# Kernel tuning notes

Measured on AMD Instinct MI355X. Metric: run time of the kernel, lower is better.

The kernel has to match this reference:

```python
import jax, jax.numpy as jnp
import numpy as np

B, S, H = 2, 4096, 1024
WINDOW = 32


def setup_inputs() -> dict:
    key = jax.random.key(0)
    ks = jax.random.split(key, 10)
    s = 1.0 / np.sqrt(H)
    return {
        "hidden_states": jax.random.normal(ks[0], (B, S, H), dtype=jnp.float32),
        "Wq": jax.random.normal(ks[1], (H, H), dtype=jnp.float32) * s,
        "Wk": jax.random.normal(ks[2], (H, H), dtype=jnp.float32) * s,
        "Wv": jax.random.normal(ks[3], (H, H), dtype=jnp.float32) * s,
        "Wo": jax.random.normal(ks[4], (H, H), dtype=jnp.float32) * s,
        "ln_w": jnp.ones((H,), dtype=jnp.float32),
        "ln_b": jnp.zeros((H,), dtype=jnp.float32),
        "W1": jax.random.normal(ks[5], (H // 2, H), dtype=jnp.float32) * s,
        "b1": jnp.zeros((H // 2,), dtype=jnp.float32),
        "W2": jax.random.normal(ks[6], (H, H // 2), dtype=jnp.float32) * (1.0 / np.sqrt(H // 2)),
        "b2": jnp.zeros((H,), dtype=jnp.float32),
    }


def _layernorm(x, w, b, eps=1e-5):
    mu = jnp.mean(x, axis=-1, keepdims=True)
    var = jnp.var(x, axis=-1, keepdims=True)
    return (x - mu) * jax.lax.rsqrt(var + eps) * w + b


def reference(hidden_states, Wq, Wk, Wv, Wo, ln_w, ln_b, W1, b1, W2, b2):
    x = hidden_states  # [B,S,H]
    q = x @ Wq.T
    k = x @ Wk.T
    v = x @ Wv.T
    # banded causal mask: keep j<=i and j >= i-WINDOW+1
    i = jnp.arange(S)[:, None]
    j = jnp.arange(S)[None, :]
    local_mask = (j <= i) & (j >= i - WINDOW + 1)  # [S,S] bool
    scores = jnp.einsum('bqh,bkh->bqk', q, k) / np.sqrt(H)
    scores = jnp.where(local_mask[None], scores, -jnp.inf)
    probs = jax.nn.softmax(scores, axis=-1)
    attn_out = jnp.einsum('bqk,bkh->bqh', probs, v) @ Wo.T
    draft = x + attn_out
    h = _layernorm(draft, ln_w, ln_b)
    h = jax.nn.gelu(h @ W1.T + b1, approximate=False)
    adapter_out = h @ W2.T + b2
    return draft + adapter_out
```

## Files before the change

kernel.cpp:

```cpp
#include <hip/hip_runtime.h>
#include <stdint.h>

typedef unsigned short u16;
typedef __bf16 bfx8 __attribute__((ext_vector_type(8)));
typedef float f32x4 __attribute__((ext_vector_type(4)));

__device__ __forceinline__ u16 f2bf(float x) {
    unsigned int u = __float_as_uint(x);
    u += 0x7fffu + ((u >> 16) & 1u);
    return (u16)(u >> 16);
}

__device__ __forceinline__ void async16(const void* g, void* l) {
    __builtin_amdgcn_global_load_lds(
        (const __attribute__((address_space(1))) unsigned int*)(uintptr_t)g,
        (__attribute__((address_space(3))) unsigned int*)(unsigned int)(uintptr_t)l,
        16, 0, 0);
}

#define S_BARRIER() asm volatile("s_barrier" ::: "memory")
#define WAIT_VM6() asm volatile("s_waitcnt vmcnt(6)" ::: "memory")
#define WAIT_VM8() asm volatile("s_waitcnt vmcnt(8)" ::: "memory")
#define WAIT_VM0() asm volatile("s_waitcnt vmcnt(0)" ::: "memory")

struct CastArgs {
    const float* src[7];
    u16* dst[7];
    int nblk[7];
};
__global__ __launch_bounds__(256) void cast_all(CastArgs a) {
    int b = blockIdx.x, seg = 0;
    while (b >= a.nblk[seg]) { b -= a.nblk[seg]; ++seg; }
    int i = b * 256 + threadIdx.x;
    const float4* p = (const float4*)(a.src[seg] + (size_t)i * 8);
    float4 x = p[0], y = p[1];
    ushort4 o0, o1;
    o0.x = f2bf(x.x); o0.y = f2bf(x.y); o0.z = f2bf(x.z); o0.w = f2bf(x.w);
    o1.x = f2bf(y.x); o1.y = f2bf(y.y); o1.z = f2bf(y.z); o1.w = f2bf(y.w);
    ushort4* q = (ushort4*)(a.dst[seg] + (size_t)i * 8);
    q[0] = o0; q[1] = o1;
}

#define QKV_LDA(SLOT, RBASE)                                                  \
    {                                                                         \
        _Pragma("unroll") for (int m = 0; m < 4; ++m) {                       \
            int r = (RBASE) + m * 16 + laneR;                                 \
            int ph = (laneK + (r >> 2)) & 3;                                  \
            af[m] = *(const bfx8*)(lds + (SLOT) + r * 64 + ph * 16);          \
        }                                                                     \
    }
#define QKV_LDB(SLOT)                                                         \
    {                                                                         \
        _Pragma("unroll") for (int n = 0; n < 4; ++n) {                       \
            int r = bBase + n * 16 + laneR;                                   \
            int ph = (laneK + (r >> 2)) & 3;                                  \
            bf[n] = *(const bfx8*)(lds + (SLOT) + r * 64 + ph * 16);          \
        }                                                                     \
    }
#define QKV_MFMA(Q)                                                           \
    __builtin_amdgcn_s_setprio(1);                                            \
    _Pragma("unroll") for (int m = 0; m < 4; ++m)                             \
        _Pragma("unroll") for (int n = 0; n < 4; ++n)                         \
            acc[(Q) + m][n] = __builtin_amdgcn_mfma_f32_16x16x32_bf16(        \
                af[m], bf[n], acc[(Q) + m][n], 0, 0, 0);                      \
    __builtin_amdgcn_s_setprio(0);

__global__ __launch_bounds__(512, 2)
void gemm_qkv(const u16* __restrict__ A, const u16* __restrict__ Bw,
              u16* __restrict__ outq, u16* __restrict__ outk,
              u16* __restrict__ vt, int K) {
    __shared__ __align__(1024) unsigned char lds[131072];
    const int t = threadIdx.x;
    const int lane = t & 63;
    const int w = t >> 6;
    const int laneR = lane & 15, laneK = lane >> 4;
    const int wm = w >> 2, wn = w & 3;
    const int b = blockIdx.x;
    const int swz = (b & 7) * 48 + (b >> 3);
    const int row0 = (swz / 12) * 256;
    const int col0 = (swz % 12) * 256;
    const int nt = K >> 6;

    const int c0 = t, c1 = 512 + t;
    const u16* pA0 = A + (size_t)(row0 + (c0 >> 2)) * K + (((c0 & 3) - (c0 >> 4)) & 3) * 8;
    const u16* pA1 = A + (size_t)(row0 + (c1 >> 2)) * K + (((c1 & 3) - (c1 >> 4)) & 3) * 8;
    const u16* pB0 = Bw + (size_t)(col0 + (c0 >> 2)) * K + (((c0 & 3) - (c0 >> 4)) & 3) * 8;
    const u16* pB1 = Bw + (size_t)(col0 + (c1 >> 2)) * K + (((c1 & 3) - (c1 >> 4)) & 3) * 8;
    const unsigned dst0 = (unsigned)c0 * 16u, dst1 = (unsigned)c1 * 16u;

    auto stageA = [&](int d, int ks, int tk) {
        unsigned base = (unsigned)d * 65536u + (unsigned)ks * 16384u;
        async16(pA0 + tk * 64 + ks * 32, lds + base + dst0);
        async16(pA1 + tk * 64 + ks * 32, lds + base + dst1);
    };
    auto stageB = [&](int d, int ks, int tk) {
        unsigned base = (unsigned)d * 65536u + 32768u + (unsigned)ks * 16384u;
        async16(pB0 + tk * 64 + ks * 32, lds + base + dst0);
        async16(pB1 + tk * 64 + ks * 32, lds + base + dst1);
    };

    stageA(0, 0, 0); stageB(0, 0, 0);
    stageA(0, 1, 0); stageB(0, 1, 0);
    stageA(1, 0, 1); stageB(1, 0, 1);
    WAIT_VM8();
    S_BARRIER();

    f32x4 acc[8][4] = {};
    const int aRow = wm * 128;
    const int bBase = wn * 64;

    for (int tk = 0; tk < nt; ++tk) {
        const unsigned d = (unsigned)(tk & 1) * 65536u;
        const int t1 = (tk + 1 < nt) ? tk + 1 : nt - 1;
        const int t2 = (tk + 2 < nt) ? tk + 2 : nt - 1;
        bfx8 af[4], bf[4];
        QKV_LDA(d, aRow)
        QKV_LDB(d + 32768u)
        stageA(t1 & 1, 1, t1);
        S_BARRIER();
        QKV_MFMA(0)
        S_BARRIER();
        QKV_LDA(d, aRow + 64)
        stageB(t1 & 1, 1, t1);
        S_BARRIER();
        QKV_MFMA(4)
        WAIT_VM8();
        S_BARRIER();
        QKV_LDA(d + 16384u, aRow)
        QKV_LDB(d + 49152u)
        stageA(t2 & 1, 0, t2);
        S_BARRIER();
        QKV_MFMA(0)
        S_BARRIER();
        QKV_LDA(d + 16384u, aRow + 64)
        stageB(t2 & 1, 0, t2);
        S_BARRIER();
        QKV_MFMA(4)
        WAIT_VM8();
        S_BARRIER();
    }
    WAIT_VM0();

    const int colsec = col0 >> 10;
#pragma unroll
    for (int mi = 0; mi < 8; ++mi) {
        const int gr0 = row0 + wm * 128 + mi * 16 + laneK * 4;
#pragma unroll
        for (int n = 0; n < 4; ++n) {
            const int gc = col0 + wn * 64 + n * 16 + laneR;
            if (colsec == 0) {
#pragma unroll
                for (int r = 0; r < 4; ++r)
                    outq[(size_t)(gr0 + r) * 1024 + gc] = f2bf(acc[mi][n][r]);
            } else if (colsec == 1) {
#pragma unroll
                for (int r = 0; r < 4; ++r)
                    outk[(size_t)(gr0 + r) * 1024 + (gc - 1024)] = f2bf(acc[mi][n][r]);
            } else {
                ushort4 o4;
                o4.x = f2bf(acc[mi][n][0]); o4.y = f2bf(acc[mi][n][1]);
                o4.z = f2bf(acc[mi][n][2]); o4.w = f2bf(acc[mi][n][3]);
                *(ushort4*)(vt + (((size_t)(gr0 >> 12)) * 1024 + (gc - 2048)) * 4096 +
                            (gr0 & 4095)) = o4;
            }
        }
    }
}

template <int EPI>
__global__ __launch_bounds__(512, 2)
void gemm_nt(const u16* __restrict__ A, const u16* __restrict__ Bw,
             u16* __restrict__ outb, float* __restrict__ outf,
             const float* __restrict__ res, const float* __restrict__ bias,
             int M, int N, int K) {
    __shared__ __align__(1024) unsigned char lds[147456];
    const int t = threadIdx.x;
    const int lane = t & 63, w = t >> 6;
    const int laneR = lane & 15, laneK = lane >> 4;
    const int wr = w >> 1, wc = w & 1;
    const int row0 = blockIdx.y * 256, col0 = blockIdx.x * 128;
    const int nt = K >> 6;

    f32x4 acc[4][4] = {};

    const u16* srcA[4];
    const u16* srcB[2];
    unsigned dA[4], dB[2];
#pragma unroll
    for (int i = 0; i < 4; ++i) {
        int li = i * 512 + t;
        int row = li >> 3, ko = li & 7;
        srcA[i] = A + (size_t)(row0 + row) * K + (ko ^ (row & 7)) * 8;
        dA[i] = li * 16;
    }
#pragma unroll
    for (int i = 0; i < 2; ++i) {
        int li = i * 512 + t;
        int row = li >> 3, ko = li & 7;
        srcB[i] = Bw + (size_t)(col0 + row) * K + (ko ^ (row & 7)) * 8;
        dB[i] = 32768 + li * 16;
    }

    auto stage = [&](int b, int tk, int h) {
        unsigned char* base = lds + b * 49152;
        const int o = tk * 64;
        if (h == 0) {
            async16(srcA[0] + o, base + dA[0]);
            async16(srcA[1] + o, base + dA[1]);
            async16(srcB[0] + o, base + dB[0]);
        } else {
            async16(srcA[2] + o, base + dA[2]);
            async16(srcA[3] + o, base + dA[3]);
            async16(srcB[1] + o, base + dB[1]);
        }
    };

    stage(0, 0, 0); stage(0, 0, 1);
    stage(1, 1, 0); stage(1, 1, 1);

    for (int tk = 0; tk < nt; ++tk) {
        unsigned char* bufA = lds + (tk % 3) * 49152;
        unsigned char* bufB = bufA + 32768;
        if (tk + 1 < nt) { WAIT_VM6(); } else { WAIT_VM0(); }
        S_BARRIER();
        const bool pf = (tk + 2 < nt);
        const int nb = (tk + 2) % 3;
#pragma unroll
        for (int ks = 0; ks < 2; ++ks) {
            bfx8 af[4], bf[4];
#pragma unroll
            for (int m = 0; m < 4; ++m) {
                int r = wr * 64 + m * 16 + laneR;
                int phys = (ks * 4 + laneK) ^ (r & 7);
                af[m] = *(const bfx8*)(bufA + r * 128 + phys * 16);
            }
#pragma unroll
            for (int n = 0; n < 4; ++n) {
                int r = wc * 64 + n * 16 + laneR;
                int phys = (ks * 4 + laneK) ^ (r & 7);
                bf[n] = *(const bfx8*)(bufB + r * 128 + phys * 16);
            }
            if (pf) stage(nb, tk + 2, ks);
            S_BARRIER();
            __builtin_amdgcn_s_setprio(1);
#pragma unroll
            for (int m = 0; m < 4; ++m)
#pragma unroll
                for (int n = 0; n < 4; ++n)
                    acc[m][n] = __builtin_amdgcn_mfma_f32_16x16x32_bf16(
                        af[m], bf[n], acc[m][n], 0, 0, 0);
            __builtin_amdgcn_s_setprio(0);
            S_BARRIER();
        }
    }

#pragma unroll
    for (int m = 0; m < 4; ++m) {
        const int gr0 = row0 + wr * 64 + m * 16 + laneK * 4;
#pragma unroll
        for (int n = 0; n < 4; ++n) {
            const int gc = col0 + wc * 64 + n * 16 + laneR;
            if constexpr (EPI == 1) {
#pragma unroll
                for (int r = 0; r < 4; ++r) {
                    size_t idx = (size_t)(gr0 + r) * N + gc;
                    outf[idx] = res[idx] + acc[m][n][r];
                }
            } else if constexpr (EPI == 2) {
#pragma unroll
                for (int r = 0; r < 4; ++r) {
                    float xx = acc[m][n][r] + bias[gc];
                    outb[(size_t)(gr0 + r) * N + gc] =
                        f2bf(xx * 0.5f * (1.0f + erff(xx * 0.70710678118654752f)));
                }
            } else {
#pragma unroll
                for (int r = 0; r < 4; ++r) {
                    size_t idx = (size_t)(gr0 + r) * N + gc;
                    outf[idx] = res[idx] + acc[m][n][r] + bias[gc];
                }
            }
        }
    }
}

__global__ __launch_bounds__(256, 2)
void attn_kernel(const u16* __restrict__ Q, const u16* __restrict__ K,
                 const u16* __restrict__ vt, u16* __restrict__ O) {
    constexpr int H = 1024, S = 4096;
    const int t = threadIdx.x, lane = t & 63, w = t >> 6;
    const int laneR = lane & 15, laneK = lane >> 4;
    const int tile = blockIdx.x;
    const int batch = tile >> 7;
    const int i0 = (tile & 127) * 32;
    const size_t base = (size_t)batch * S * H;

    __shared__ __align__(16) float S4[4][32][64];
    __shared__ __align__(16) u16 P[32][72];

    f32x4 sc[2][4] = {};
    for (int h = w * 256; h < w * 256 + 256; h += 32) {
        bfx8 qa[2];
#pragma unroll
        for (int m = 0; m < 2; ++m) {
            size_t row = (size_t)(i0 + m * 16 + laneR);
            qa[m] = *(const bfx8*)(Q + base + row * H + h + laneK * 8);
        }
        bfx8 kb[4];
#pragma unroll
        for (int n = 0; n < 4; ++n) {
            int j = i0 - 32 + n * 16 + laneR;
            int jc = j < 0 ? 0 : j;
            kb[n] = *(const bfx8*)(K + base + (size_t)jc * H + h + laneK * 8);
        }
#pragma unroll
        for (int m = 0; m < 2; ++m)
#pragma unroll
            for (int n = 0; n < 4; ++n)
                sc[m][n] = __builtin_amdgcn_mfma_f32_16x16x32_bf16(
                    qa[m], kb[n], sc[m][n], 0, 0, 0);
    }
#pragma unroll
    for (int m = 0; m < 2; ++m)
#pragma unroll
        for (int n = 0; n < 4; ++n)
#pragma unroll
            for (int r = 0; r < 4; ++r)
                S4[w][m * 16 + laneK * 4 + r][n * 16 + laneR] = sc[m][n][r];
    __syncthreads();

    {
        int q = t >> 3;
        int c0 = (t & 7) * 8;
        int lo = q + 1;
        if (32 - i0 > lo) lo = 32 - i0;
        int hi = q + 32;
        float vals[8];
        float mx = -1e30f;
#pragma unroll
        for (int c = 0; c < 8; ++c) {
            int cc = c0 + c;
            float v = (S4[0][q][cc] + S4[1][q][cc] + S4[2][q][cc] + S4[3][q][cc]) * 0.03125f;
            bool valid = (cc >= lo) && (cc <= hi);
            vals[c] = valid ? v : -1e30f;
            if (vals[c] > mx) mx = vals[c];
        }
#pragma unroll
        for (int d = 1; d < 8; d <<= 1) {
            float o = __shfl_xor(mx, d);
            if (o > mx) mx = o;
        }
        float sum = 0.f;
        float es[8];
#pragma unroll
        for (int c = 0; c < 8; ++c) {
            es[c] = (vals[c] > -1e29f) ? __expf(vals[c] - mx) : 0.f;
            sum += es[c];
        }
#pragma unroll
        for (int d = 1; d < 8; d <<= 1) sum += __shfl_xor(sum, d);
        float inv = 1.0f / sum;
#pragma unroll
        for (int c = 0; c < 8; ++c) P[q][c0 + c] = f2bf(es[c] * inv);
    }
    __syncthreads();

    for (int nc = 0; nc < 4; ++nc) {
        int ncol = w * 256 + nc * 64;
        f32x4 o[2][4] = {};
#pragma unroll
        for (int ks = 0; ks < 2; ++ks) {
            bfx8 pa[2];
#pragma unroll
            for (int m = 0; m < 2; ++m)
                pa[m] = *(const bfx8*)(&P[m * 16 + laneR][ks * 32 + laneK * 8]);
            int t0 = i0 - 32 + ks * 32 + laneK * 8;
            if (t0 < 0) t0 = 0;
#pragma unroll
            for (int n = 0; n < 4; ++n) {
                int c = ncol + n * 16 + laneR;
                bfx8 vb = *(const bfx8*)(vt + ((size_t)batch * 1024 + c) * 4096 + t0);
#pragma unroll
                for (int m = 0; m < 2; ++m)
                    o[m][n] = __builtin_amdgcn_mfma_f32_16x16x32_bf16(
                        pa[m], vb, o[m][n], 0, 0, 0);
            }
        }
#pragma unroll
        for (int m = 0; m < 2; ++m)
#pragma unroll
            for (int n = 0; n < 4; ++n)
#pragma unroll
                for (int r = 0; r < 4; ++r) {
                    size_t row = (size_t)(i0 + m * 16 + laneK * 4 + r);
                    O[base + row * H + ncol + n * 16 + laneR] = f2bf(o[m][n][r]);
                }
    }
}

__global__ __launch_bounds__(256)
void ln_kernel(const float* __restrict__ x, const float* __restrict__ gw,
               const float* __restrict__ gb, u16* __restrict__ out) {
    const int row = blockIdx.x, t = threadIdx.x;
    const float4 v = ((const float4*)(x + (size_t)row * 1024))[t];
    float s = v.x + v.y + v.z + v.w;
    float s2 = v.x * v.x + v.y * v.y + v.z * v.z + v.w * v.w;
#pragma unroll
    for (int d = 1; d < 64; d <<= 1) {
        s += __shfl_xor(s, d);
        s2 += __shfl_xor(s2, d);
    }
    __shared__ float red[8];
    int lane = t & 63, wv = t >> 6;
    if (lane == 0) { red[wv] = s; red[4 + wv] = s2; }
    __syncthreads();
    float S1 = red[0] + red[1] + red[2] + red[3];
    float S2 = red[4] + red[5] + red[6] + red[7];
    float mu = S1 * (1.0f / 1024.0f);
    float var = S2 * (1.0f / 1024.0f) - mu * mu;
    float rstd = rsqrtf(var + 1e-5f);
    const float4 wv4 = ((const float4*)gw)[t];
    const float4 bv4 = ((const float4*)gb)[t];
    ushort4 o;
    o.x = f2bf((v.x - mu) * rstd * wv4.x + bv4.x);
    o.y = f2bf((v.y - mu) * rstd * wv4.y + bv4.y);
    o.z = f2bf((v.z - mu) * rstd * wv4.z + bv4.z);
    o.w = f2bf((v.w - mu) * rstd * wv4.w + bv4.w);
    ((ushort4*)(out + (size_t)row * 1024))[t] = o;
}

extern "C" void kernel_launch(void* const* d_in, const int* in_sizes, int n_in,
                              void* d_out, int out_size, void* d_ws, size_t ws_size,
                              hipStream_t stream) {
    const float* x   = (const float*)d_in[0];
    const float* Wq  = (const float*)d_in[1];
    const float* Wk  = (const float*)d_in[2];
    const float* Wv  = (const float*)d_in[3];
    const float* Wo  = (const float*)d_in[4];
    const float* lnw = (const float*)d_in[5];
    const float* lnb = (const float*)d_in[6];
    const float* W1  = (const float*)d_in[7];
    const float* b1  = (const float*)d_in[8];
    const float* W2  = (const float*)d_in[9];
    const float* b2  = (const float*)d_in[10];
    (void)in_sizes; (void)n_in; (void)out_size; (void)ws_size;

    const int M = 8192, H = 1024, Hh = 512;

    char* ws = (char*)d_ws;
    size_t off = 0;
    auto alloc = [&](size_t bytes) {
        char* p = ws + off;
        off += (bytes + 255) & ~(size_t)255;
        return p;
    };
    u16* Xb    = (u16*)alloc((size_t)M * H * 2);
    u16* Wqkvb = (u16*)alloc((size_t)3 * H * H * 2);
    u16* Wob   = (u16*)alloc((size_t)H * H * 2);
    u16* W1b   = (u16*)alloc((size_t)Hh * H * 2);
    u16* W2b   = (u16*)alloc((size_t)H * Hh * 2);
    u16* Qb    = (u16*)alloc((size_t)M * H * 2);
    u16* Kb    = (u16*)alloc((size_t)M * H * 2);
    u16* Vt    = (u16*)alloc((size_t)M * H * 2);
    float* draft = (float*)alloc((size_t)M * H * 4);
    u16* Attb = Xb;
    u16* hlnb = Qb;
    u16* Gb   = Kb;
    float* outp = (float*)d_out;

    CastArgs ca;
    ca.src[0] = x;  ca.dst[0] = Xb;                        ca.nblk[0] = (M * H / 8) / 256;
    ca.src[1] = Wq; ca.dst[1] = Wqkvb;                     ca.nblk[1] = (H * H / 8) / 256;
    ca.src[2] = Wk; ca.dst[2] = Wqkvb + (size_t)H * H;     ca.nblk[2] = (H * H / 8) / 256;
    ca.src[3] = Wv; ca.dst[3] = Wqkvb + (size_t)2 * H * H; ca.nblk[3] = (H * H / 8) / 256;
    ca.src[4] = Wo; ca.dst[4] = Wob;                       ca.nblk[4] = (H * H / 8) / 256;
    ca.src[5] = W1; ca.dst[5] = W1b;                       ca.nblk[5] = (Hh * H / 8) / 256;
    ca.src[6] = W2; ca.dst[6] = W2b;                       ca.nblk[6] = (H * Hh / 8) / 256;
    int totblk = 0;
    for (int i = 0; i < 7; ++i) totblk += ca.nblk[i];
    cast_all<<<dim3(totblk), dim3(256), 0, stream>>>(ca);

    gemm_qkv<<<dim3(384), dim3(512), 0, stream>>>(Xb, Wqkvb, Qb, Kb, Vt, H);

    attn_kernel<<<dim3(256), dim3(256), 0, stream>>>(Qb, Kb, Vt, Attb);

    gemm_nt<1><<<dim3(H / 128, M / 256), dim3(512), 0, stream>>>(
        Attb, Wob, nullptr, draft, x, nullptr, M, H, H);

    ln_kernel<<<dim3(M), dim3(256), 0, stream>>>(draft, lnw, lnb, hlnb);

    gemm_nt<2><<<dim3(Hh / 128, M / 256), dim3(512), 0, stream>>>(
        hlnb, W1b, Gb, nullptr, nullptr, b1, M, Hh, H);

    gemm_nt<3><<<dim3(H / 128, M / 256), dim3(512), 0, stream>>>(
        Gb, W2b, nullptr, outp, draft, b2, M, H, Hh);
}
```

Measured before the change: 196.8 us.

## Restructure QKV GEMM LDS layout to 128-byte rows with XOR swizzle and single-tile prefetch

Changes the QKV GEMM shared-memory layout from two 32-wide k-slices per tile to full 64-wide rows of 128 bytes with an XOR swizzle. Each k-tile is now prefetched as a whole into the alternate buffer during the first half of the current tile, replacing the previous staggered half-tile staging. The intent is to cut LDS bank conflicts and simplify the async-load/wait schedule. The trade-off is a shallower prefetch distance, and the vmcnt thresholds must exactly match the number of outstanding loads.

```diff
diff --git a/kernel.cpp b/kernel.cpp
--- a/kernel.cpp
+++ b/kernel.cpp
@@ -20,7 +20,8 @@
 
 #define S_BARRIER() asm volatile("s_barrier" ::: "memory")
 #define WAIT_VM6() asm volatile("s_waitcnt vmcnt(6)" ::: "memory")
-#define WAIT_VM8() asm volatile("s_waitcnt vmcnt(8)" ::: "memory")
+#define WAIT_VM4() asm volatile("s_waitcnt vmcnt(4)" ::: "memory")
+#define WAIT_VM2() asm volatile("s_waitcnt vmcnt(2)" ::: "memory")
 #define WAIT_VM0() asm volatile("s_waitcnt vmcnt(0)" ::: "memory")
 
 struct CastArgs {
@@ -41,38 +42,13 @@
     q[0] = o0; q[1] = o1;
 }
 
-#define QKV_LDA(SLOT, RBASE)                                                  \
-    {                                                                         \
-        _Pragma("unroll") for (int m = 0; m < 4; ++m) {                       \
-            int r = (RBASE) + m * 16 + laneR;                                 \
-            int ph = (laneK + (r >> 2)) & 3;                                  \
-            af[m] = *(const bfx8*)(lds + (SLOT) + r * 64 + ph * 16);          \
-        }                                                                     \
-    }
-#define QKV_LDB(SLOT)                                                         \
-    {                                                                         \
-        _Pragma("unroll") for (int n = 0; n < 4; ++n) {                       \
-            int r = bBase + n * 16 + laneR;                                   \
-            int ph = (laneK + (r >> 2)) & 3;                                  \
-            bf[n] = *(const bfx8*)(lds + (SLOT) + r * 64 + ph * 16);          \
-        }                                                                     \
-    }
-#define QKV_MFMA(Q)                                                           \
-    __builtin_amdgcn_s_setprio(1);                                            \
-    _Pragma("unroll") for (int m = 0; m < 4; ++m)                             \
-        _Pragma("unroll") for (int n = 0; n < 4; ++n)                         \
-            acc[(Q) + m][n] = __builtin_amdgcn_mfma_f32_16x16x32_bf16(        \
-                af[m], bf[n], acc[(Q) + m][n], 0, 0, 0);                      \
-    __builtin_amdgcn_s_setprio(0);
-
 __global__ __launch_bounds__(512, 2)
 void gemm_qkv(const u16* __restrict__ A, const u16* __restrict__ Bw,
               u16* __restrict__ outq, u16* __restrict__ outk,
               u16* __restrict__ vt, int K) {
     __shared__ __align__(1024) unsigned char lds[131072];
     const int t = threadIdx.x;
-    const int lane = t & 63;
-    const int w = t >> 6;
+    const int lane = t & 63, w = t >> 6;
     const int laneR = lane & 15, laneK = lane >> 4;
     const int wm = w >> 2, wn = w & 3;
     const int b = blockIdx.x;
@@ -81,62 +57,89 @@
     const int col0 = (swz % 12) * 256;
     const int nt = K >> 6;
 
-    const int c0 = t, c1 = 512 + t;
-    const u16* pA0 = A + (size_t)(row0 + (c0 >> 2)) * K + (((c0 & 3) - (c0 >> 4)) & 3) * 8;
-    const u16* pA1 = A + (size_t)(row0 + (c1 >> 2)) * K + (((c1 & 3) - (c1 >> 4)) & 3) * 8;
-    const u16* pB0 = Bw + (size_t)(col0 + (c0 >> 2)) * K + (((c0 & 3) - (c0 >> 4)) & 3) * 8;
-    const u16* pB1 = Bw + (size_t)(col0 + (c1 >> 2)) * K + (((c1 & 3) - (c1 >> 4)) & 3) * 8;
-    const unsigned dst0 = (unsigned)c0 * 16u, dst1 = (unsigned)c1 * 16u;
-
-    auto stageA = [&](int d, int ks, int tk) {
-        unsigned base = (unsigned)d * 65536u + (unsigned)ks * 16384u;
-        async16(pA0 + tk * 64 + ks * 32, lds + base + dst0);
-        async16(pA1 + tk * 64 + ks * 32, lds + base + dst1);
-    };
-    auto stageB = [&](int d, int ks, int tk) {
-        unsigned base = (unsigned)d * 65536u + 32768u + (unsigned)ks * 16384u;
-        async16(pB0 + tk * 64 + ks * 32, lds + base + dst0);
-        async16(pB1 + tk * 64 + ks * 32, lds + base + dst1);
-    };
-
-    stageA(0, 0, 0); stageB(0, 0, 0);
-    stageA(0, 1, 0); stageB(0, 1, 0);
-    stageA(1, 0, 1); stageB(1, 0, 1);
-    WAIT_VM8();
+    const u16* pA[2][2];
+    const u16* pB[2][2];
+#pragma unroll
+    for (int u = 0; u < 2; ++u)
+#pragma unroll
+        for (int j = 0; j < 2; ++j) {
+            int c = u * 1024 + j * 512 + t;
+            int row = c >> 3;
+            int ko = (c & 7) ^ (row & 7);
+            pA[u][j] = A + (size_t)(row0 + row) * K + ko * 8;
+            pB[u][j] = Bw + (size_t)(col0 + row) * K + ko * 8;
+        }
+
+    auto stageA = [&](unsigned d, int u, int tk) {
+        async16(pA[u][0] + tk * 64, lds + d + (u * 1024 + t) * 16);
+        async16(pA[u][1] + tk * 64, lds + d + (u * 1024 + 512 + t) * 16);
+    };
+    auto stageB = [&](unsigned d, int u, int tk) {
+        async16(pB[u][0] + tk * 64, lds + d + 32768u + (u * 1024 + t) * 16);
+        async16(pB[u][1] + tk * 64, lds + d + 32768u + (u * 1024 + 512 + t) * 16);
+    };
+
+    f32x4 acc[8][4] = {};
+    const int aR = wm * 128;
+    const int bR = wn * 64;
+    bfx8 af[4], bf[4];
+
+    auto LDA = [&](unsigned d, int ks, int half) {
+#pragma unroll
+        for (int m = 0; m < 4; ++m) {
+            int r = aR + half * 64 + m * 16 + laneR;
+            int ph = (ks * 4 + laneK) ^ (r & 7);
+            af[m] = *(const bfx8*)(lds + d + r * 128 + ph * 16);
+        }
+    };
+    auto LDB = [&](unsigned d, int ks) {
+#pragma unroll
+        for (int n = 0; n < 4; ++n) {
+            int r = bR + n * 16 + laneR;
+            int ph = (ks * 4 + laneK) ^ (r & 7);
+            bf[n] = *(const bfx8*)(lds + d + 32768u + r * 128 + ph * 16);
+        }
+    };
+    auto DOMFMA = [&](int off) {
+        __builtin_amdgcn_s_setprio(1);
+#pragma unroll
+        for (int m = 0; m < 4; ++m)
+#pragma unroll
+            for (int n = 0; n < 4; ++n)
+                acc[off + m][n] = __builtin_amdgcn_mfma_f32_16x16x32_bf16(
+                    af[m], bf[n], acc[off + m][n], 0, 0, 0);
+        __builtin_amdgcn_s_setprio(0);
+    };
+
+    stageA(0, 0, 0); stageB(0, 0, 0); stageB(0, 1, 0); stageA(0, 1, 0);
+    WAIT_VM0();
     S_BARRIER();
-
-    f32x4 acc[8][4] = {};
-    const int aRow = wm * 128;
-    const int bBase = wn * 64;
 
     for (int tk = 0; tk < nt; ++tk) {
         const unsigned d = (unsigned)(tk & 1) * 65536u;
-        const int t1 = (tk + 1 < nt) ? tk + 1 : nt - 1;
-        const int t2 = (tk + 2 < nt) ? tk + 2 : nt - 1;
-        bfx8 af[4], bf[4];
-        QKV_LDA(d, aRow)
-        QKV_LDB(d + 32768u)
-        stageA(t1 & 1, 1, t1);
-        S_BARRIER();
-        QKV_MFMA(0)
-        S_BARRIER();
-        QKV_LDA(d, aRow + 64)
-        stageB(t1 & 1, 1, t1);
-        S_BARRIER();
-        QKV_MFMA(4)
-        WAIT_VM8();
-        S_BARRIER();
-        QKV_LDA(d + 16384u, aRow)
-        QKV_LDB(d + 49152u)
-        stageA(t2 & 1, 0, t2);
-        S_BARRIER();
-        QKV_MFMA(0)
-        S_BARRIER();
-        QKV_LDA(d + 16384u, aRow + 64)
-        stageB(t2 & 1, 0, t2);
-        S_BARRIER();
-        QKV_MFMA(4)
-        WAIT_VM8();
+        const unsigned nd = d ^ 65536u;
+        const bool pf = (tk + 1 < nt);
+        LDA(d, 0, 0);
+        LDB(d, 0);
+        if (pf) { stageA(nd, 0, tk + 1); stageB(nd, 0, tk + 1); }
+        S_BARRIER();
+        DOMFMA(0);
+        WAIT_VM4();
+        S_BARRIER();
+        LDA(d, 0, 1);
+        if (pf) { stageB(nd, 1, tk + 1); stageA(nd, 1, tk + 1); }
+        S_BARRIER();
+        DOMFMA(4);
+        S_BARRIER();
+        LDA(d, 1, 0);
+        LDB(d, 1);
+        S_BARRIER();
+        DOMFMA(0);
+        S_BARRIER();
+        LDA(d, 1, 1);
+        S_BARRIER();
+        DOMFMA(4);
+        WAIT_VM2();
         S_BARRIER();
     }
     WAIT_VM0();
```

New measurement: 192.1 us. -2.4%, faster.
